# Kernel tuning notes

Measured on AMD Instinct MI355X. Metric: run time of the kernel, lower is better.

## Reference

```python
import jax, jax.numpy as jnp
import numpy as np

B, T, F = 4096, 256, 64
ANN_IN, OUT = 128, 32
U = [128, 128]


def setup_inputs() -> dict:
    key = jax.random.key(0)
    ks = jax.random.split(key, 8)
    s = 0.05  # weight scale for numerical sanity
    return {
        "inputs": jax.random.normal(ks[0], (B, T, F), jnp.float32),
        "W_in": jax.random.normal(ks[1], (F + OUT, ANN_IN), jnp.float32) * s,
        "b_in": jnp.zeros((ANN_IN,), jnp.float32),
        "k0": jax.random.normal(ks[2], (ANN_IN, 4 * U[0]), jnp.float32) * s,
        "rk0": jax.random.normal(ks[3], (U[0], 4 * U[0]), jnp.float32) * s,
        "bb0": jnp.zeros((4 * U[0],), jnp.float32),
        "k1": jax.random.normal(ks[4], (U[0], 4 * U[1]), jnp.float32) * s,
        "rk1": jax.random.normal(ks[5], (U[1], 4 * U[1]), jnp.float32) * s,
        "bb1": jnp.zeros((4 * U[1],), jnp.float32),
        "W_out": jax.random.normal(ks[6], (U[1], OUT), jnp.float32) * s,
        "b_out": jnp.zeros((OUT,), jnp.float32),
    }


def _lstm_cell(x, h, c, k, rk, b):
    # Keras LSTMCell: z = x@k + h@rk + b, split into i,f,g,o
    z = x @ k + h @ rk + b
    i, f, g, o = jnp.split(z, 4, axis=-1)
    c_new = jax.nn.sigmoid(f) * c + jax.nn.sigmoid(i) * jnp.tanh(g)
    h_new = jax.nn.sigmoid(o) * jnp.tanh(c_new)
    return h_new, c_new


def reference(inputs, W_in, b_in, k0, rk0, bb0, k1, rk1, bb1, W_out, b_out):
    b = inputs.shape[0]
    dt = inputs.dtype
    u0, u1 = rk0.shape[0], rk1.shape[0]
    out_units = W_out.shape[1]

    def step(carry, x_t):
        acc, h0, c0, h1, c1 = carry
        a = jnp.concatenate([x_t, acc], axis=-1) @ W_in + b_in  # ann_in Dense (linear)
        h0, c0 = _lstm_cell(a, h0, c0, k0, rk0, bb0)
        h1, c1 = _lstm_cell(h0, h1, c1, k1, rk1, bb1)
        res = h1 @ W_out + b_out  # ann_out Dense (linear)
        acc = acc + res  # explicit discrete integration
        return (acc, h0, c0, h1, c1), res

    init = (
        jnp.zeros((b, out_units), dt),
        jnp.zeros((b, u0), dt), jnp.zeros((b, u0), dt),
        jnp.zeros((b, u1), dt), jnp.zeros((b, u1), dt),
    )
    xs = jnp.swapaxes(inputs, 0, 1)  # [T, B, F]
    _, outs = jax.lax.scan(step, init, xs)
    return jnp.swapaxes(outs, 0, 1)  # [B, T, OUT] per-step residuals (cell outputs)
```

## Files before the change

kernel.cpp:

```cpp
#include <hip/hip_runtime.h>
#include <hip/hip_fp16.h>

typedef _Float16 half8  __attribute__((ext_vector_type(8)));
typedef _Float16 half2v __attribute__((ext_vector_type(2)));
typedef float    f32x4  __attribute__((ext_vector_type(4)));

#define MFMA16(af, bf, cf) __builtin_amdgcn_mfma_f32_16x16x32_f16((af), (bf), (cf), 0, 0, 0)

#define WS_WL1  0
#define WS_RK0  131072
#define WS_W0   (131072 + 65536)
#define WS_WOUT (WS_W0 + 49152)
#define WS_B0   (WS_WOUT + 4096)

#define PA0 104
#define PH  136
#define L_A0   0
#define L_H0   3328
#define L_H1   (L_H0 + 4352)
#define L_WOUT (L_H1 + 4352)
#define L_K1   (L_WOUT + 4096)
#define L_TOT  (L_K1 + 65536)

__device__ __forceinline__ float sigm(float x) {
    return __builtin_amdgcn_rcpf(1.0f + __builtin_amdgcn_exp2f(-1.442695041f * x));
}
__device__ __forceinline__ float tanh_(float x) {
    return 1.0f - 2.0f * __builtin_amdgcn_rcpf(__builtin_amdgcn_exp2f(2.885390082f * x) + 1.0f);
}
__device__ __forceinline__ void bar() {
    asm volatile("s_waitcnt lgkmcnt(0)" ::: "memory");
    __builtin_amdgcn_s_barrier();
    asm volatile("" ::: "memory");
}


__global__ void pack_layer_k(const float* __restrict__ kk, const float* __restrict__ rk,
                             _Float16* __restrict__ dst)
{
    int idx  = blockIdx.x * 256 + threadIdx.x;
    int j    = idx & 7;
    int lane = (idx >> 3) & 63;
    int fk   = idx >> 9;
    int kt   = fk & 7;
    int nt   = fk >> 3;
    int w = nt >> 3, ln = nt & 7, g = ln >> 1, hh = ln & 1;
    int col = g*128 + w*32 + hh*16 + (lane & 15);
    int row = kt*32 + (lane >> 4)*8 + j;
    float v = (row < 128) ? kk[row*512 + col] : rk[(row - 128)*512 + col];
    dst[idx] = (_Float16)v;
}

__global__ void pack_rk(const float* __restrict__ rk, _Float16* __restrict__ dst)
{
    int idx = blockIdx.x * 256 + threadIdx.x;
    int j = idx & 7, lane = (idx >> 3) & 63, fk = idx >> 9;
    int kt = fk & 3, nt = fk >> 2;
    int w = nt >> 3, ln = nt & 7, g = ln >> 1, hh = ln & 1;
    int col = g*128 + w*32 + hh*16 + (lane & 15);
    int row = kt*32 + (lane >> 4)*8 + j;
    dst[idx] = (_Float16)rk[row*512 + col];
}

__global__ void pack_w0(const float* __restrict__ W_in, const float* __restrict__ k0,
                        _Float16* __restrict__ dst)
{
    int idx = blockIdx.x * 256 + threadIdx.x;
    int j = idx & 7, lane = (idx >> 3) & 63, fk = idx >> 9;
    int kt = fk % 3, nt = fk / 3;
    int w = nt >> 3, ln = nt & 7, g = ln >> 1, hh = ln & 1;
    int col = g*128 + w*32 + hh*16 + (lane & 15);
    int row = kt*32 + (lane >> 4)*8 + j;
    float s = 0.f;
    #pragma unroll 4
    for (int k = 0; k < 128; ++k) s += W_in[row*128 + k] * k0[k*512 + col];
    dst[idx] = (_Float16)s;
}

__global__ void pack_b0(const float* __restrict__ b_in, const float* __restrict__ k0,
                        const float* __restrict__ bb0, float* __restrict__ b0p)
{
    int col = blockIdx.x * 256 + threadIdx.x;
    float s = bb0[col];
    #pragma unroll 4
    for (int k = 0; k < 128; ++k) s += b_in[k] * k0[k*512 + col];
    b0p[col] = s;
}

__global__ void pack_wout(const float* __restrict__ W_out, _Float16* __restrict__ dst)
{
    int idx = blockIdx.x * 256 + threadIdx.x;
    int j = idx & 7, lane = (idx >> 3) & 63, fk = idx >> 9;
    int kt = fk & 3, nt = fk >> 2;
    int col = nt*16 + (lane & 15);
    int row = kt*32 + (lane >> 4)*8 + j;
    dst[idx] = (_Float16)W_out[row*32 + col];
}

__global__ __launch_bounds__(512, 2)
void acclstm_main(const float* __restrict__ xin,
                  const _Float16* __restrict__ wl1p, const _Float16* __restrict__ rk0p,
                  const _Float16* __restrict__ w0p,  const _Float16* __restrict__ woutp,
                  const float* __restrict__ b0p, const float* __restrict__ bb1,
                  const float* __restrict__ bout, float* __restrict__ out)
{
    __shared__ __align__(16) _Float16 lds[L_TOT];
    const int tid  = threadIdx.x;
    const int W    = tid >> 6;
    const int lane = tid & 63;
    const int w4   = W & 3;
    const int hh   = W >> 2;
    const int l15  = lane & 15;
    const int lg   = lane >> 4;
    const int b0   = blockIdx.x << 4;
    const int colw = w4*32 + hh*16 + l15;

    for (int i = tid; i < 8192; i += 512) {
        int h = i << 3, nt = h >> 11, rem = h & 2047;
        *reinterpret_cast<uint4*>(&lds[L_K1 + h]) =
            *reinterpret_cast<const uint4*>(&wl1p[nt*4096 + rem]);
    }
    *reinterpret_cast<uint4*>(&lds[L_WOUT + (tid << 3)]) =
        *reinterpret_cast<const uint4*>(&woutp[tid << 3]);
    {
        uint4 z; z.x = z.y = z.z = z.w = 0u;
        for (int i = tid; i < 1504; i += 512)
            *reinterpret_cast<uint4*>(&lds[i << 3]) = z;
    }

    half8 w0r[4][3], rk0r[4][4], rk1r[4][4];
    #pragma unroll
    for (int g = 0; g < 4; ++g) {
        const int nt = w4*8 + g*2 + hh;
        #pragma unroll
        for (int kt = 0; kt < 3; ++kt)
            w0r[g][kt] = *reinterpret_cast<const half8*>(&w0p[(nt*3 + kt)*512 + lane*8]);
        #pragma unroll
        for (int kt = 0; kt < 4; ++kt)
            rk0r[g][kt] = *reinterpret_cast<const half8*>(&rk0p[(nt*4 + kt)*512 + lane*8]);
        #pragma unroll
        for (int kt = 0; kt < 4; ++kt)
            rk1r[g][kt] = *reinterpret_cast<const half8*>(&wl1p[(nt*8 + 4 + kt)*512 + lane*8]);
    }
    float b0v[4], b1v[4];
    #pragma unroll
    for (int g = 0; g < 4; ++g) {
        b0v[g] = b0p[g*128 + colw];
        b1v[g] = bb1[g*128 + colw];
    }
    const float boutv = (W < 2) ? bout[W*16 + l15] : 0.0f;

    f32x4 c0 = {0.f,0.f,0.f,0.f}, c1 = {0.f,0.f,0.f,0.f}, accv = {0.f,0.f,0.f,0.f};

    const int xrow = tid >> 5, xc2 = (tid & 31) << 1;
    __syncthreads();
    float2 xr = *reinterpret_cast<const float2*>(&xin[(size_t)(b0 + xrow)*16384 + xc2]);
    {
        half2v xh = { (_Float16)xr.x, (_Float16)xr.y };
        *reinterpret_cast<half2v*>(&lds[L_A0 + xrow*PA0 + xc2]) = xh;
    }
    xr = *reinterpret_cast<const float2*>(&xin[(size_t)(b0 + xrow)*16384 + 64 + xc2]);
    __syncthreads();

    auto step = [&](auto PARc, int t) {
        constexpr int PAR = decltype(PARc)::value;
        constexpr int A0r = L_A0 + PAR*1664,       A0w = L_A0 + (PAR^1)*1664;
        constexpr int H0r = L_H0 + PAR*2176,       H0w = L_H0 + (PAR^1)*2176;
        constexpr int H1r = L_H1 + PAR*2176,       H1w = L_H1 + (PAR^1)*2176;

        {
            f32x4 z0={0.f,0.f,0.f,0.f}, z1={0.f,0.f,0.f,0.f};
            f32x4 z2={0.f,0.f,0.f,0.f}, z3={0.f,0.f,0.f,0.f};
            #pragma unroll
            for (int kt = 0; kt < 3; ++kt) {
                half8 af = *reinterpret_cast<const half8*>(&lds[A0r + l15*PA0 + kt*32 + lg*8]);
                z0 = MFMA16(af, w0r[0][kt], z0);
                z1 = MFMA16(af, w0r[1][kt], z1);
                z2 = MFMA16(af, w0r[2][kt], z2);
                z3 = MFMA16(af, w0r[3][kt], z3);
            }
            #pragma unroll
            for (int kt = 0; kt < 4; ++kt) {
                half8 af = *reinterpret_cast<const half8*>(&lds[H0r + l15*PH + kt*32 + lg*8]);
                z0 = MFMA16(af, rk0r[0][kt], z0);
                z1 = MFMA16(af, rk0r[1][kt], z1);
                z2 = MFMA16(af, rk0r[2][kt], z2);
                z3 = MFMA16(af, rk0r[3][kt], z3);
            }
            #pragma unroll
            for (int r = 0; r < 4; ++r) {
                float iv = sigm (z0[r] + b0v[0]);
                float fv = sigm (z1[r] + b0v[1]);
                float gv = tanh_(z2[r] + b0v[2]);
                float ov = sigm (z3[r] + b0v[3]);
                float cn = fv * c0[r] + iv * gv;
                c0[r] = cn;
                lds[H0w + (lg*4 + r)*PH + colw] = (_Float16)(ov * tanh_(cn));
            }
        }
        bar();

        {
            f32x4 z0={0.f,0.f,0.f,0.f}, z1={0.f,0.f,0.f,0.f};
            f32x4 z2={0.f,0.f,0.f,0.f}, z3={0.f,0.f,0.f,0.f};
            #pragma unroll
            for (int kt = 0; kt < 4; ++kt) {
                half8 af = *reinterpret_cast<const half8*>(&lds[H0w + l15*PH + kt*32 + lg*8]);
                z0 = MFMA16(af, *reinterpret_cast<const half8*>(&lds[L_K1 + ((w4*8 + 0 + hh)*4 + kt)*512 + lane*8]), z0);
                z1 = MFMA16(af, *reinterpret_cast<const half8*>(&lds[L_K1 + ((w4*8 + 2 + hh)*4 + kt)*512 + lane*8]), z1);
                z2 = MFMA16(af, *reinterpret_cast<const half8*>(&lds[L_K1 + ((w4*8 + 4 + hh)*4 + kt)*512 + lane*8]), z2);
                z3 = MFMA16(af, *reinterpret_cast<const half8*>(&lds[L_K1 + ((w4*8 + 6 + hh)*4 + kt)*512 + lane*8]), z3);
            }
            #pragma unroll
            for (int kt = 0; kt < 4; ++kt) {
                half8 af = *reinterpret_cast<const half8*>(&lds[H1r + l15*PH + kt*32 + lg*8]);
                z0 = MFMA16(af, rk1r[0][kt], z0);
                z1 = MFMA16(af, rk1r[1][kt], z1);
                z2 = MFMA16(af, rk1r[2][kt], z2);
                z3 = MFMA16(af, rk1r[3][kt], z3);
            }
            #pragma unroll
            for (int r = 0; r < 4; ++r) {
                float iv = sigm (z0[r] + b1v[0]);
                float fv = sigm (z1[r] + b1v[1]);
                float gv = tanh_(z2[r] + b1v[2]);
                float ov = sigm (z3[r] + b1v[3]);
                float cn = fv * c1[r] + iv * gv;
                c1[r] = cn;
                lds[H1w + (lg*4 + r)*PH + colw] = (_Float16)(ov * tanh_(cn));
            }
        }
        bar();

        if (W < 2) {
            f32x4 rr = {0.f,0.f,0.f,0.f};
            #pragma unroll
            for (int kt = 0; kt < 4; ++kt) {
                half8 af = *reinterpret_cast<const half8*>(&lds[H1w + l15*PH + kt*32 + lg*8]);
                half8 wf = *reinterpret_cast<const half8*>(&lds[L_WOUT + (W*4 + kt)*512 + lane*8]);
                rr = MFMA16(af, wf, rr);
            }
            #pragma unroll
            for (int r = 0; r < 4; ++r) {
                float res = rr[r] + boutv;
                out[(size_t)(b0 + lg*4 + r)*8192 + t*32 + W*16 + l15] = res;
                accv[r] += res;
                lds[A0w + (lg*4 + r)*PA0 + 64 + W*16 + l15] = (_Float16)accv[r];
            }
        }
        {
            half2v xh = { (_Float16)xr.x, (_Float16)xr.y };
            *reinterpret_cast<half2v*>(&lds[A0w + xrow*PA0 + xc2]) = xh;
            int tn = t + 2; if (tn > 255) tn = 255;
            xr = *reinterpret_cast<const float2*>(&xin[(size_t)(b0 + xrow)*16384 + tn*64 + xc2]);
        }
        bar();
    };

    #pragma unroll 1
    for (int t = 0; t < 256; t += 2) {
        step(std::integral_constant<int,0>{}, t);
        step(std::integral_constant<int,1>{}, t + 1);
    }
}

extern "C" void kernel_launch(void* const* d_in, const int* in_sizes, int n_in,
                              void* d_out, int out_size, void* d_ws, size_t ws_size,
                              hipStream_t stream) {
    (void)in_sizes; (void)n_in; (void)out_size; (void)ws_size;
    const float* x     = (const float*)d_in[0];
    const float* W_in  = (const float*)d_in[1];
    const float* b_in  = (const float*)d_in[2];
    const float* k0    = (const float*)d_in[3];
    const float* rk0   = (const float*)d_in[4];
    const float* bb0   = (const float*)d_in[5];
    const float* k1    = (const float*)d_in[6];
    const float* rk1   = (const float*)d_in[7];
    const float* bb1   = (const float*)d_in[8];
    const float* W_out = (const float*)d_in[9];
    const float* b_out = (const float*)d_in[10];
    float* out = (float*)d_out;

    _Float16* ws    = (_Float16*)d_ws;
    _Float16* wl1p  = ws + WS_WL1;
    _Float16* rk0p  = ws + WS_RK0;
    _Float16* w0p   = ws + WS_W0;
    _Float16* woutp = ws + WS_WOUT;
    float*    b0p   = (float*)(ws + WS_B0);

    pack_layer_k<<<512, 256, 0, stream>>>(k1, rk1, wl1p);
    pack_rk     <<<256, 256, 0, stream>>>(rk0, rk0p);
    pack_w0     <<<192, 256, 0, stream>>>(W_in, k0, w0p);
    pack_b0     <<<2,   256, 0, stream>>>(b_in, k0, bb0, b0p);
    pack_wout   <<<16,  256, 0, stream>>>(W_out, woutp);
    acclstm_main<<<256, 512, 0, stream>>>(x, wl1p, rk0p, w0p, woutp,
                                          b0p, bb1, b_out, out);
}
```

Baseline: 780.5 us.

## Fold accumulator into layer-0 gate preactivation and merge output projection into layer 0 phase

```diff
diff --git a/kernel.cpp b/kernel.cpp
--- a/kernel.cpp
+++ b/kernel.cpp
@@ -7,20 +7,23 @@
 
 #define MFMA16(af, bf, cf) __builtin_amdgcn_mfma_f32_16x16x32_f16((af), (bf), (cf), 0, 0, 0)
 
-#define WS_WL1  0
-#define WS_RK0  131072
-#define WS_W0   (131072 + 65536)
-#define WS_WOUT (WS_W0 + 49152)
-#define WS_B0   (WS_WOUT + 4096)
-
-#define PA0 104
+#define WS_WL1   0
+#define WS_RK0   131072
+#define WS_W0    (131072 + 65536)
+#define WS_WOUTT (WS_W0 + 49152)
+#define WS_B0    (WS_WOUTT + 4096)
+#define WS_CB    (WS_B0 + 1024)
+
+#define PA0 72
 #define PH  136
-#define L_A0   0
-#define L_H0   3328
+#define PRES 40
+#define L_A0X  0
+#define L_H0   2304
 #define L_H1   (L_H0 + 4352)
-#define L_WOUT (L_H1 + 4352)
-#define L_K1   (L_WOUT + 4096)
-#define L_TOT  (L_K1 + 65536)
+#define L_RES  (L_H1 + 4352)
+#define L_WOUTT (L_RES + 5120)
+#define L_K1   (L_WOUTT + 4096)
+#define L_TOT  (L_K1 + 49152)
 
 __device__ __forceinline__ float sigm(float x) {
     return __builtin_amdgcn_rcpf(1.0f + __builtin_amdgcn_exp2f(-1.442695041f * x));
@@ -33,7 +36,6 @@
     __builtin_amdgcn_s_barrier();
     asm volatile("" ::: "memory");
 }
-
 
 __global__ void pack_layer_k(const float* __restrict__ kk, const float* __restrict__ rk,
                              _Float16* __restrict__ dst)
@@ -87,22 +89,37 @@
     b0p[col] = s;
 }
 
-__global__ void pack_wout(const float* __restrict__ W_out, _Float16* __restrict__ dst)
+__global__ void pack_woutT(const float* __restrict__ W_out, _Float16* __restrict__ dst)
 {
     int idx = blockIdx.x * 256 + threadIdx.x;
     int j = idx & 7, lane = (idx >> 3) & 63, fk = idx >> 9;
-    int kt = fk & 3, nt = fk >> 2;
-    int col = nt*16 + (lane & 15);
+    int kt = fk & 3, m = fk >> 2;
     int row = kt*32 + (lane >> 4)*8 + j;
+    int col = m*16 + (lane & 15);
     dst[idx] = (_Float16)W_out[row*32 + col];
+}
+
+__global__ void pack_cb(const float* __restrict__ W_in, const float* __restrict__ k0,
+                        const float* __restrict__ bout, float* __restrict__ cbp)
+{
+    int zc = blockIdx.x * 256 + threadIdx.x;
+    float s = 0.f;
+    for (int c = 0; c < 32; ++c) {
+        float wv = 0.f;
+        #pragma unroll 4
+        for (int k = 0; k < 128; ++k) wv += W_in[(64 + c)*128 + k] * k0[k*512 + zc];
+        s += bout[c] * wv;
+    }
+    cbp[zc] = s;
 }
 
 __global__ __launch_bounds__(512, 2)
 void acclstm_main(const float* __restrict__ xin,
                   const _Float16* __restrict__ wl1p, const _Float16* __restrict__ rk0p,
-                  const _Float16* __restrict__ w0p,  const _Float16* __restrict__ woutp,
-                  const float* __restrict__ b0p, const float* __restrict__ bb1,
-                  const float* __restrict__ bout, float* __restrict__ out)
+                  const _Float16* __restrict__ w0p,  const _Float16* __restrict__ woutTp,
+                  const float* __restrict__ b0p, const float* __restrict__ cbp,
+                  const float* __restrict__ bb1, const float* __restrict__ bout,
+                  float* __restrict__ out)
 {
     __shared__ __align__(16) _Float16 lds[L_TOT];
     const int tid  = threadIdx.x;
@@ -114,138 +131,136 @@
     const int lg   = lane >> 4;
     const int b0   = blockIdx.x << 4;
     const int colw = w4*32 + hh*16 + l15;
-
-    for (int i = tid; i < 8192; i += 512) {
-        int h = i << 3, nt = h >> 11, rem = h & 2047;
+    const int nt0 = w4*8 + 0 + hh, nt1 = w4*8 + 2 + hh, nt2 = w4*8 + 4 + hh, nt3 = w4*8 + 6 + hh;
+
+    for (int i = tid; i < 6144; i += 512) {
+        int h = i << 3, nt = h / 1536, rem = h % 1536;
         *reinterpret_cast<uint4*>(&lds[L_K1 + h]) =
             *reinterpret_cast<const uint4*>(&wl1p[nt*4096 + rem]);
     }
-    *reinterpret_cast<uint4*>(&lds[L_WOUT + (tid << 3)]) =
-        *reinterpret_cast<const uint4*>(&woutp[tid << 3]);
+    *reinterpret_cast<uint4*>(&lds[L_WOUTT + (tid << 3)]) =
+        *reinterpret_cast<const uint4*>(&woutTp[tid << 3]);
     {
         uint4 z; z.x = z.y = z.z = z.w = 0u;
-        for (int i = tid; i < 1504; i += 512)
-            *reinterpret_cast<uint4*>(&lds[i << 3]) = z;
-    }
-
-    half8 w0r[4][3], rk0r[4][4], rk1r[4][4];
+        if (tid < 272) {
+            *reinterpret_cast<uint4*>(&lds[L_H0 + (tid << 3)]) = z;
+            *reinterpret_cast<uint4*>(&lds[L_H1 + (tid << 3)]) = z;
+        }
+    }
+
+    half8 rk0r[4][4], rk1r[4][4], k1r[4], w0a[4];
+    {
+        const int nts[4] = {nt0, nt1, nt2, nt3};
+        #pragma unroll
+        for (int g = 0; g < 4; ++g) {
+            const int nt = nts[g];
+            #pragma unroll
+            for (int kt = 0; kt < 4; ++kt)
+                rk0r[g][kt] = *reinterpret_cast<const half8*>(&rk0p[(nt*4 + kt)*512 + lane*8]);
+            #pragma unroll
+            for (int kt = 0; kt < 4; ++kt)
+                rk1r[g][kt] = *reinterpret_cast<const half8*>(&wl1p[(nt*8 + 4 + kt)*512 + lane*8]);
+            k1r[g] = *reinterpret_cast<const half8*>(&wl1p[(nt*8 + 3)*512 + lane*8]);
+            w0a[g] = *reinterpret_cast<const half8*>(&w0p[(nt*3 + 2)*512 + lane*8]);
+        }
+    }
+    float b1v[4], cbv[4];
+    f32x4 za[4];
     #pragma unroll
     for (int g = 0; g < 4; ++g) {
-        const int nt = w4*8 + g*2 + hh;
-        #pragma unroll
-        for (int kt = 0; kt < 3; ++kt)
-            w0r[g][kt] = *reinterpret_cast<const half8*>(&w0p[(nt*3 + kt)*512 + lane*8]);
-        #pragma unroll
-        for (int kt = 0; kt < 4; ++kt)
-            rk0r[g][kt] = *reinterpret_cast<const half8*>(&rk0p[(nt*4 + kt)*512 + lane*8]);
-        #pragma unroll
-        for (int kt = 0; kt < 4; ++kt)
-            rk1r[g][kt] = *reinterpret_cast<const half8*>(&wl1p[(nt*8 + 4 + kt)*512 + lane*8]);
-    }
-    float b0v[4], b1v[4];
+        b1v[g] = bb1[g*128 + colw];
+        cbv[g] = cbp[g*128 + colw];
+        float z0i = b0p[g*128 + colw] - cbv[g];
+        za[g] = (f32x4){z0i, z0i, z0i, z0i};
+    }
+    float boutv4[4];
     #pragma unroll
-    for (int g = 0; g < 4; ++g) {
-        b0v[g] = b0p[g*128 + colw];
-        b1v[g] = bb1[g*128 + colw];
-    }
-    const float boutv = (W < 2) ? bout[W*16 + l15] : 0.0f;
-
-    f32x4 c0 = {0.f,0.f,0.f,0.f}, c1 = {0.f,0.f,0.f,0.f}, accv = {0.f,0.f,0.f,0.f};
+    for (int r = 0; r < 4; ++r)
+        boutv4[r] = bout[(W < 2 ? W : 0)*16 + lg*4 + r];
+
+    f32x4 c0 = {0.f,0.f,0.f,0.f}, c1 = {0.f,0.f,0.f,0.f};
 
     const int xrow = tid >> 5, xc2 = (tid & 31) << 1;
+    const int resw = L_RES + W*640 + l15*PRES;
+
     __syncthreads();
     float2 xr = *reinterpret_cast<const float2*>(&xin[(size_t)(b0 + xrow)*16384 + xc2]);
     {
         half2v xh = { (_Float16)xr.x, (_Float16)xr.y };
-        *reinterpret_cast<half2v*>(&lds[L_A0 + xrow*PA0 + xc2]) = xh;
+        *reinterpret_cast<half2v*>(&lds[L_A0X + xrow*PA0 + xc2]) = xh;
     }
     xr = *reinterpret_cast<const float2*>(&xin[(size_t)(b0 + xrow)*16384 + 64 + xc2]);
     __syncthreads();
 
     auto step = [&](auto PARc, int t) {
         constexpr int PAR = decltype(PARc)::value;
-        constexpr int A0r = L_A0 + PAR*1664,       A0w = L_A0 + (PAR^1)*1664;
-        constexpr int H0r = L_H0 + PAR*2176,       H0w = L_H0 + (PAR^1)*2176;
-        constexpr int H1r = L_H1 + PAR*2176,       H1w = L_H1 + (PAR^1)*2176;
+        constexpr int A0r = L_A0X + PAR*1152, A0w = L_A0X + (PAR^1)*1152;
+        constexpr int H0r = L_H0 + PAR*2176,  H0w = L_H0 + (PAR^1)*2176;
+        constexpr int H1r = L_H1 + PAR*2176,  H1w = L_H1 + (PAR^1)*2176;
 
         {
-            f32x4 z0={0.f,0.f,0.f,0.f}, z1={0.f,0.f,0.f,0.f};
-            f32x4 z2={0.f,0.f,0.f,0.f}, z3={0.f,0.f,0.f,0.f};
-            #pragma unroll
-            for (int kt = 0; kt < 3; ++kt) {
-                half8 af = *reinterpret_cast<const half8*>(&lds[A0r + l15*PA0 + kt*32 + lg*8]);
-                z0 = MFMA16(af, w0r[0][kt], z0);
-                z1 = MFMA16(af, w0r[1][kt], z1);
-                z2 = MFMA16(af, w0r[2][kt], z2);
-                z3 = MFMA16(af, w0r[3][kt], z3);
-            }
+            f32x4 rr0 = {0.f,0.f,0.f,0.f}, rr1 = {0.f,0.f,0.f,0.f};
             #pragma unroll
             for (int kt = 0; kt < 4; ++kt) {
-                half8 af = *reinterpret_cast<const half8*>(&lds[H0r + l15*PH + kt*32 + lg*8]);
-                z0 = MFMA16(af, rk0r[0][kt], z0);
-                z1 = MFMA16(af, rk0r[1][kt], z1);
-                z2 = MFMA16(af, rk0r[2][kt], z2);
-                z3 = MFMA16(af, rk0r[3][kt], z3);
+                half8 hf  = *reinterpret_cast<const half8*>(&lds[H1r + l15*PH + kt*32 + lg*8]);
+                half8 wt0 = *reinterpret_cast<const half8*>(&lds[L_WOUTT + (0*4 + kt)*512 + lane*8]);
+                half8 wt1 = *reinterpret_cast<const half8*>(&lds[L_WOUTT + (1*4 + kt)*512 + lane*8]);
+                rr0 = MFMA16(wt0, hf, rr0);
+                rr1 = MFMA16(wt1, hf, rr1);
             }
             #pragma unroll
             for (int r = 0; r < 4; ++r) {
-                float iv = sigm (z0[r] + b0v[0]);
-                float fv = sigm (z1[r] + b0v[1]);
-                float gv = tanh_(z2[r] + b0v[2]);
-                float ov = sigm (z3[r] + b0v[3]);
+                lds[resw + lg*4 + r]      = (_Float16)rr0[r];
+                lds[resw + 16 + lg*4 + r] = (_Float16)rr1[r];
+            }
+            asm volatile("s_waitcnt lgkmcnt(0)" ::: "memory");
+            half8 resA = *reinterpret_cast<const half8*>(&lds[resw + lg*8]);
+            #pragma unroll
+            for (int g = 0; g < 4; ++g) {
+                za[g] = MFMA16(resA, w0a[g], za[g]);
+                #pragma unroll
+                for (int r = 0; r < 4; ++r) za[g][r] += cbv[g];
+            }
+            if (t && W < 2) {
+                const f32x4& rrs = (W == 0) ? rr0 : rr1;
+                #pragma unroll
+                for (int r = 0; r < 4; ++r)
+                    out[(size_t)(b0 + l15)*8192 + (t-1)*32 + W*16 + lg*4 + r] = rrs[r] + boutv4[r];
+            }
+        }
+
+        {
+            half8 ax0 = *reinterpret_cast<const half8*>(&lds[A0r + l15*PA0 +  0 + lg*8]);
+            half8 ax1 = *reinterpret_cast<const half8*>(&lds[A0r + l15*PA0 + 32 + lg*8]);
+            half8 wx00 = *reinterpret_cast<const half8*>(&w0p[(nt0*3 + 0)*512 + lane*8]);
+            half8 wx01 = *reinterpret_cast<const half8*>(&w0p[(nt0*3 + 1)*512 + lane*8]);
+            half8 wx10 = *reinterpret_cast<const half8*>(&w0p[(nt1*3 + 0)*512 + lane*8]);
+            half8 wx11 = *reinterpret_cast<const half8*>(&w0p[(nt1*3 + 1)*512 + lane*8]);
+            half8 wx20 = *reinterpret_cast<const half8*>(&w0p[(nt2*3 + 0)*512 + lane*8]);
+            half8 wx21 = *reinterpret_cast<const half8*>(&w0p[(nt2*3 + 1)*512 + lane*8]);
+            half8 wx30 = *reinterpret_cast<const half8*>(&w0p[(nt3*3 + 0)*512 + lane*8]);
+            half8 wx31 = *reinterpret_cast<const half8*>(&w0p[(nt3*3 + 1)*512 + lane*8]);
+            f32x4 z0 = MFMA16(ax0, wx00, za[0]); z0 = MFMA16(ax1, wx01, z0);
+            f32x4 z1 = MFMA16(ax0, wx10, za[1]); z1 = MFMA16(ax1, wx11, z1);
+            f32x4 z2 = MFMA16(ax0, wx20, za[2]); z2 = MFMA16(ax1, wx21, z2);
+            f32x4 z3 = MFMA16(ax0, wx30, za[3]); z3 = MFMA16(ax1, wx31, z3);
+            #pragma unroll
+            for (int kt = 0; kt < 4; ++kt) {
+                half8 hf = *reinterpret_cast<const half8*>(&lds[H0r + l15*PH + kt*32 + lg*8]);
+                z0 = MFMA16(hf, rk0r[0][kt], z0);
+                z1 = MFMA16(hf, rk0r[1][kt], z1);
+                z2 = MFMA16(hf, rk0r[2][kt], z2);
+                z3 = MFMA16(hf, rk0r[3][kt], z3);
+            }
+            #pragma unroll
+            for (int r = 0; r < 4; ++r) {
+                float iv = sigm (z0[r]);
+                float fv = sigm (z1[r]);
+                float gv = tanh_(z2[r]);
+                float ov = sigm (z3[r]);
                 float cn = fv * c0[r] + iv * gv;
                 c0[r] = cn;
                 lds[H0w + (lg*4 + r)*PH + colw] = (_Float16)(ov * tanh_(cn));
-            }
-        }
-        bar();
-
-        {
-            f32x4 z0={0.f,0.f,0.f,0.f}, z1={0.f,0.f,0.f,0.f};
-            f32x4 z2={0.f,0.f,0.f,0.f}, z3={0.f,0.f,0.f,0.f};
-            #pragma unroll
-            for (int kt = 0; kt < 4; ++kt) {
-                half8 af = *reinterpret_cast<const half8*>(&lds[H0w + l15*PH + kt*32 + lg*8]);
-                z0 = MFMA16(af, *reinterpret_cast<const half8*>(&lds[L_K1 + ((w4*8 + 0 + hh)*4 + kt)*512 + lane*8]), z0);
-                z1 = MFMA16(af, *reinterpret_cast<const half8*>(&lds[L_K1 + ((w4*8 + 2 + hh)*4 + kt)*512 + lane*8]), z1);
-                z2 = MFMA16(af, *reinterpret_cast<const half8*>(&lds[L_K1 + ((w4*8 + 4 + hh)*4 + kt)*512 + lane*8]), z2);
-                z3 = MFMA16(af, *reinterpret_cast<const half8*>(&lds[L_K1 + ((w4*8 + 6 + hh)*4 + kt)*512 + lane*8]), z3);
-            }
-            #pragma unroll
-            for (int kt = 0; kt < 4; ++kt) {
-                half8 af = *reinterpret_cast<const half8*>(&lds[H1r + l15*PH + kt*32 + lg*8]);
-                z0 = MFMA16(af, rk1r[0][kt], z0);
-                z1 = MFMA16(af, rk1r[1][kt], z1);
-                z2 = MFMA16(af, rk1r[2][kt], z2);
-                z3 = MFMA16(af, rk1r[3][kt], z3);
-            }
-            #pragma unroll
-            for (int r = 0; r < 4; ++r) {
-                float iv = sigm (z0[r] + b1v[0]);
-                float fv = sigm (z1[r] + b1v[1]);
-                float gv = tanh_(z2[r] + b1v[2]);
-                float ov = sigm (z3[r] + b1v[3]);
-                float cn = fv * c1[r] + iv * gv;
-                c1[r] = cn;
-                lds[H1w + (lg*4 + r)*PH + colw] = (_Float16)(ov * tanh_(cn));
-            }
-        }
-        bar();
-
-        if (W < 2) {
-            f32x4 rr = {0.f,0.f,0.f,0.f};
-            #pragma unroll
-            for (int kt = 0; kt < 4; ++kt) {
-                half8 af = *reinterpret_cast<const half8*>(&lds[H1w + l15*PH + kt*32 + lg*8]);
-                half8 wf = *reinterpret_cast<const half8*>(&lds[L_WOUT + (W*4 + kt)*512 + lane*8]);
-                rr = MFMA16(af, wf, rr);
-            }
-            #pragma unroll
-            for (int r = 0; r < 4; ++r) {
-                float res = rr[r] + boutv;
-                out[(size_t)(b0 + lg*4 + r)*8192 + t*32 + W*16 + l15] = res;
-                accv[r] += res;
-                lds[A0w + (lg*4 + r)*PA0 + 64 + W*16 + l15] = (_Float16)accv[r];
             }
         }
         {
@@ -255,12 +270,71 @@
             xr = *reinterpret_cast<const float2*>(&xin[(size_t)(b0 + xrow)*16384 + tn*64 + xc2]);
         }
         bar();
+
+        {
+            f32x4 z0 = {b1v[0],b1v[0],b1v[0],b1v[0]};
+            f32x4 z1 = {b1v[1],b1v[1],b1v[1],b1v[1]};
+            f32x4 z2 = {b1v[2],b1v[2],b1v[2],b1v[2]};
+            f32x4 z3 = {b1v[3],b1v[3],b1v[3],b1v[3]};
+            #pragma unroll
+            for (int kt = 0; kt < 3; ++kt) {
+                half8 hf = *reinterpret_cast<const half8*>(&lds[H0w + l15*PH + kt*32 + lg*8]);
+                z0 = MFMA16(hf, *reinterpret_cast<const half8*>(&lds[L_K1 + (nt0*3 + kt)*512 + lane*8]), z0);
+                z1 = MFMA16(hf, *reinterpret_cast<const half8*>(&lds[L_K1 + (nt1*3 + kt)*512 + lane*8]), z1);
+                z2 = MFMA16(hf, *reinterpret_cast<const half8*>(&lds[L_K1 + (nt2*3 + kt)*512 + lane*8]), z2);
+                z3 = MFMA16(hf, *reinterpret_cast<const half8*>(&lds[L_K1 + (nt3*3 + kt)*512 + lane*8]), z3);
+            }
+            {
+                half8 hf = *reinterpret_cast<const half8*>(&lds[H0w + l15*PH + 3*32 + lg*8]);
+                z0 = MFMA16(hf, k1r[0], z0);
+                z1 = MFMA16(hf, k1r[1], z1);
+                z2 = MFMA16(hf, k1r[2], z2);
+                z3 = MFMA16(hf, k1r[3], z3);
+            }
+            #pragma unroll
+            for (int kt = 0; kt < 4; ++kt) {
+                half8 hf = *reinterpret_cast<const half8*>(&lds[H1r + l15*PH + kt*32 + lg*8]);
+                z0 = MFMA16(hf, rk1r[0][kt], z0);
+                z1 = MFMA16(hf, rk1r[1][kt], z1);
+                z2 = MFMA16(hf, rk1r[2][kt], z2);
+                z3 = MFMA16(hf, rk1r[3][kt], z3);
+            }
+            #pragma unroll
+            for (int r = 0; r < 4; ++r) {
+                float iv = sigm (z0[r]);
+                float fv = sigm (z1[r]);
+                float gv = tanh_(z2[r]);
+                float ov = sigm (z3[r]);
+                float cn = fv * c1[r] + iv * gv;
+                c1[r] = cn;
+                lds[H1w + (lg*4 + r)*PH + colw] = (_Float16)(ov * tanh_(cn));
+            }
+        }
+        bar();
     };
 
     #pragma unroll 1
     for (int t = 0; t < 256; t += 2) {
         step(std::integral_constant<int,0>{}, t);
         step(std::integral_constant<int,1>{}, t + 1);
+    }
+
+    {
+        f32x4 rr0 = {0.f,0.f,0.f,0.f}, rr1 = {0.f,0.f,0.f,0.f};
+        #pragma unroll
+        for (int kt = 0; kt < 4; ++kt) {
+            half8 hf  = *reinterpret_cast<const half8*>(&lds[L_H1 + l15*PH + kt*32 + lg*8]);
+            half8 wt0 = *reinterpret_cast<const half8*>(&lds[L_WOUTT + (0*4 + kt)*512 + lane*8]);
+            half8 wt1 = *reinterpret_cast<const half8*>(&lds[L_WOUTT + (1*4 + kt)*512 + lane*8]);
+            rr0 = MFMA16(wt0, hf, rr0);
+            rr1 = MFMA16(wt1, hf, rr1);
+        }
+        if (W < 2) {
+            const f32x4& rrs = (W == 0) ? rr0 : rr1;
+            #pragma unroll
+            for (int r = 0; r < 4; ++r)
+                out[(size_t)(b0 + l15)*8192 + 255*32 + W*16 + lg*4 + r] = rrs[r] + boutv4[r];
+        }
     }
 }
 
@@ -281,18 +355,20 @@
     const float* b_out = (const float*)d_in[10];
     float* out = (float*)d_out;
 
-    _Float16* ws    = (_Float16*)d_ws;
-    _Float16* wl1p  = ws + WS_WL1;
-    _Float16* rk0p  = ws + WS_RK0;
-    _Float16* w0p   = ws + WS_W0;
-    _Float16* woutp = ws + WS_WOUT;
-    float*    b0p   = (float*)(ws + WS_B0);
+    _Float16* ws     = (_Float16*)d_ws;
+    _Float16* wl1p   = ws + WS_WL1;
+    _Float16* rk0p   = ws + WS_RK0;
+    _Float16* w0p    = ws + WS_W0;
+    _Float16* woutTp = ws + WS_WOUTT;
+    float*    b0p    = (float*)(ws + WS_B0);
+    float*    cbp    = (float*)(ws + WS_CB);
 
     pack_layer_k<<<512, 256, 0, stream>>>(k1, rk1, wl1p);
     pack_rk     <<<256, 256, 0, stream>>>(rk0, rk0p);
     pack_w0     <<<192, 256, 0, stream>>>(W_in, k0, w0p);
     pack_b0     <<<2,   256, 0, stream>>>(b_in, k0, bb0, b0p);
-    pack_wout   <<<16,  256, 0, stream>>>(W_out, woutp);
-    acclstm_main<<<256, 512, 0, stream>>>(x, wl1p, rk0p, w0p, woutp,
-                                          b0p, bb1, b_out, out);
-}
+    pack_woutT  <<<16,  256, 0, stream>>>(W_out, woutTp);
+    pack_cb     <<<2,   256, 0, stream>>>(W_in, k0, b_out, cbp);
+    acclstm_main<<<256, 512, 0, stream>>>(x, wl1p, rk0p, w0p, woutTp,
+                                          b0p, cbp, bb1, b_out, out);
+}
```

New measurement: 1.575 ms. 2.02x slower.

## Load inputs directly into MFMA fragments and shrink LDS staging to acc

Applied to the files above, without the earlier changes.

```diff
diff --git a/kernel.cpp b/kernel.cpp
--- a/kernel.cpp
+++ b/kernel.cpp
@@ -2,7 +2,6 @@
 #include <hip/hip_fp16.h>
 
 typedef _Float16 half8  __attribute__((ext_vector_type(8)));
-typedef _Float16 half2v __attribute__((ext_vector_type(2)));
 typedef float    f32x4  __attribute__((ext_vector_type(4)));
 
 #define MFMA16(af, bf, cf) __builtin_amdgcn_mfma_f32_16x16x32_f16((af), (bf), (cf), 0, 0, 0)
@@ -13,10 +12,10 @@
 #define WS_WOUT (WS_W0 + 49152)
 #define WS_B0   (WS_WOUT + 4096)
 
-#define PA0 104
-#define PH  136
-#define L_A0   0
-#define L_H0   3328
+#define PACC 40
+#define PH   136
+#define L_ACC  0
+#define L_H0   1280
 #define L_H1   (L_H0 + 4352)
 #define L_WOUT (L_H1 + 4352)
 #define L_K1   (L_WOUT + 4096)
@@ -33,7 +32,6 @@
     __builtin_amdgcn_s_barrier();
     asm volatile("" ::: "memory");
 }
-
 
 __global__ void pack_layer_k(const float* __restrict__ kk, const float* __restrict__ rk,
                              _Float16* __restrict__ dst)
@@ -124,17 +122,21 @@
         *reinterpret_cast<const uint4*>(&woutp[tid << 3]);
     {
         uint4 z; z.x = z.y = z.z = z.w = 0u;
-        for (int i = tid; i < 1504; i += 512)
-            *reinterpret_cast<uint4*>(&lds[i << 3]) = z;
-    }
-
-    half8 w0r[4][3], rk0r[4][4], rk1r[4][4];
+        if (tid < 272) {
+            *reinterpret_cast<uint4*>(&lds[L_H0 + (tid << 3)]) = z;
+            *reinterpret_cast<uint4*>(&lds[L_H1 + (tid << 3)]) = z;
+        }
+        if (tid < 160)
+            *reinterpret_cast<uint4*>(&lds[L_ACC + (tid << 3)]) = z;
+    }
+
+    half8 w0r[4][2], w0a[4], rk0r[4][4], rk1r[4][4];
     #pragma unroll
     for (int g = 0; g < 4; ++g) {
         const int nt = w4*8 + g*2 + hh;
-        #pragma unroll
-        for (int kt = 0; kt < 3; ++kt)
-            w0r[g][kt] = *reinterpret_cast<const half8*>(&w0p[(nt*3 + kt)*512 + lane*8]);
+        w0r[g][0] = *reinterpret_cast<const half8*>(&w0p[(nt*3 + 0)*512 + lane*8]);
+        w0r[g][1] = *reinterpret_cast<const half8*>(&w0p[(nt*3 + 1)*512 + lane*8]);
+        w0a[g]    = *reinterpret_cast<const half8*>(&w0p[(nt*3 + 2)*512 + lane*8]);
         #pragma unroll
         for (int kt = 0; kt < 4; ++kt)
             rk0r[g][kt] = *reinterpret_cast<const half8*>(&rk0p[(nt*4 + kt)*512 + lane*8]);
@@ -152,47 +154,51 @@
 
     f32x4 c0 = {0.f,0.f,0.f,0.f}, c1 = {0.f,0.f,0.f,0.f}, accv = {0.f,0.f,0.f,0.f};
 
-    const int xrow = tid >> 5, xc2 = (tid & 31) << 1;
-    __syncthreads();
-    float2 xr = *reinterpret_cast<const float2*>(&xin[(size_t)(b0 + xrow)*16384 + xc2]);
-    {
-        half2v xh = { (_Float16)xr.x, (_Float16)xr.y };
-        *reinterpret_cast<half2v*>(&lds[L_A0 + xrow*PA0 + xc2]) = xh;
-    }
-    xr = *reinterpret_cast<const float2*>(&xin[(size_t)(b0 + xrow)*16384 + 64 + xc2]);
+    const float* xrow = xin + (size_t)(b0 + l15)*16384 + lg*8;
+    float4 xq0, xq1, xq2, xq3;
+    xq0 = *reinterpret_cast<const float4*>(xrow + 0);
+    xq1 = *reinterpret_cast<const float4*>(xrow + 4);
+    xq2 = *reinterpret_cast<const float4*>(xrow + 32);
+    xq3 = *reinterpret_cast<const float4*>(xrow + 36);
+
     __syncthreads();
 
     auto step = [&](auto PARc, int t) {
         constexpr int PAR = decltype(PARc)::value;
-        constexpr int A0r = L_A0 + PAR*1664,       A0w = L_A0 + (PAR^1)*1664;
-        constexpr int H0r = L_H0 + PAR*2176,       H0w = L_H0 + (PAR^1)*2176;
-        constexpr int H1r = L_H1 + PAR*2176,       H1w = L_H1 + (PAR^1)*2176;
+        constexpr int ACCr = L_ACC + PAR*640, ACCw = L_ACC + (PAR^1)*640;
+        constexpr int H0r = L_H0 + PAR*2176,  H0w = L_H0 + (PAR^1)*2176;
+        constexpr int H1r = L_H1 + PAR*2176,  H1w = L_H1 + (PAR^1)*2176;
 
         {
-            f32x4 z0={0.f,0.f,0.f,0.f}, z1={0.f,0.f,0.f,0.f};
-            f32x4 z2={0.f,0.f,0.f,0.f}, z3={0.f,0.f,0.f,0.f};
-            #pragma unroll
-            for (int kt = 0; kt < 3; ++kt) {
-                half8 af = *reinterpret_cast<const half8*>(&lds[A0r + l15*PA0 + kt*32 + lg*8]);
-                z0 = MFMA16(af, w0r[0][kt], z0);
-                z1 = MFMA16(af, w0r[1][kt], z1);
-                z2 = MFMA16(af, w0r[2][kt], z2);
-                z3 = MFMA16(af, w0r[3][kt], z3);
-            }
+            half8 aac = *reinterpret_cast<const half8*>(&lds[ACCr + l15*PACC + lg*8]);
+            f32x4 z0 = {b0v[0],b0v[0],b0v[0],b0v[0]};
+            f32x4 z1 = {b0v[1],b0v[1],b0v[1],b0v[1]};
+            f32x4 z2 = {b0v[2],b0v[2],b0v[2],b0v[2]};
+            f32x4 z3 = {b0v[3],b0v[3],b0v[3],b0v[3]};
             #pragma unroll
             for (int kt = 0; kt < 4; ++kt) {
-                half8 af = *reinterpret_cast<const half8*>(&lds[H0r + l15*PH + kt*32 + lg*8]);
-                z0 = MFMA16(af, rk0r[0][kt], z0);
-                z1 = MFMA16(af, rk0r[1][kt], z1);
-                z2 = MFMA16(af, rk0r[2][kt], z2);
-                z3 = MFMA16(af, rk0r[3][kt], z3);
-            }
+                half8 hf = *reinterpret_cast<const half8*>(&lds[H0r + l15*PH + kt*32 + lg*8]);
+                z0 = MFMA16(hf, rk0r[0][kt], z0);
+                z1 = MFMA16(hf, rk0r[1][kt], z1);
+                z2 = MFMA16(hf, rk0r[2][kt], z2);
+                z3 = MFMA16(hf, rk0r[3][kt], z3);
+            }
+            half8 ax0 = { (_Float16)xq0.x, (_Float16)xq0.y, (_Float16)xq0.z, (_Float16)xq0.w,
+                          (_Float16)xq1.x, (_Float16)xq1.y, (_Float16)xq1.z, (_Float16)xq1.w };
+            half8 ax1 = { (_Float16)xq2.x, (_Float16)xq2.y, (_Float16)xq2.z, (_Float16)xq2.w,
+                          (_Float16)xq3.x, (_Float16)xq3.y, (_Float16)xq3.z, (_Float16)xq3.w };
+            z0 = MFMA16(ax0, w0r[0][0], z0); z1 = MFMA16(ax0, w0r[1][0], z1);
+            z2 = MFMA16(ax0, w0r[2][0], z2); z3 = MFMA16(ax0, w0r[3][0], z3);
+            z0 = MFMA16(ax1, w0r[0][1], z0); z1 = MFMA16(ax1, w0r[1][1], z1);
+            z2 = MFMA16(ax1, w0r[2][1], z2); z3 = MFMA16(ax1, w0r[3][1], z3);
+            z0 = MFMA16(aac, w0a[0], z0);    z1 = MFMA16(aac, w0a[1], z1);
+            z2 = MFMA16(aac, w0a[2], z2);    z3 = MFMA16(aac, w0a[3], z3);
             #pragma unroll
             for (int r = 0; r < 4; ++r) {
-                float iv = sigm (z0[r] + b0v[0]);
-                float fv = sigm (z1[r] + b0v[1]);
-                float gv = tanh_(z2[r] + b0v[2]);
-                float ov = sigm (z3[r] + b0v[3]);
+                float iv = sigm (z0[r]);
+                float fv = sigm (z1[r]);
+                float gv = tanh_(z2[r]);
+                float ov = sigm (z3[r]);
                 float cn = fv * c0[r] + iv * gv;
                 c0[r] = cn;
                 lds[H0w + (lg*4 + r)*PH + colw] = (_Float16)(ov * tanh_(cn));
@@ -201,30 +207,32 @@
         bar();
 
         {
-            f32x4 z0={0.f,0.f,0.f,0.f}, z1={0.f,0.f,0.f,0.f};
-            f32x4 z2={0.f,0.f,0.f,0.f}, z3={0.f,0.f,0.f,0.f};
+            f32x4 z0 = {b1v[0],b1v[0],b1v[0],b1v[0]};
+            f32x4 z1 = {b1v[1],b1v[1],b1v[1],b1v[1]};
+            f32x4 z2 = {b1v[2],b1v[2],b1v[2],b1v[2]};
+            f32x4 z3 = {b1v[3],b1v[3],b1v[3],b1v[3]};
             #pragma unroll
             for (int kt = 0; kt < 4; ++kt) {
-                half8 af = *reinterpret_cast<const half8*>(&lds[H0w + l15*PH + kt*32 + lg*8]);
-                z0 = MFMA16(af, *reinterpret_cast<const half8*>(&lds[L_K1 + ((w4*8 + 0 + hh)*4 + kt)*512 + lane*8]), z0);
-                z1 = MFMA16(af, *reinterpret_cast<const half8*>(&lds[L_K1 + ((w4*8 + 2 + hh)*4 + kt)*512 + lane*8]), z1);
-                z2 = MFMA16(af, *reinterpret_cast<const half8*>(&lds[L_K1 + ((w4*8 + 4 + hh)*4 + kt)*512 + lane*8]), z2);
-                z3 = MFMA16(af, *reinterpret_cast<const half8*>(&lds[L_K1 + ((w4*8 + 6 + hh)*4 + kt)*512 + lane*8]), z3);
+                half8 hf = *reinterpret_cast<const half8*>(&lds[H0w + l15*PH + kt*32 + lg*8]);
+                z0 = MFMA16(hf, *reinterpret_cast<const half8*>(&lds[L_K1 + ((w4*8 + 0 + hh)*4 + kt)*512 + lane*8]), z0);
+                z1 = MFMA16(hf, *reinterpret_cast<const half8*>(&lds[L_K1 + ((w4*8 + 2 + hh)*4 + kt)*512 + lane*8]), z1);
+                z2 = MFMA16(hf, *reinterpret_cast<const half8*>(&lds[L_K1 + ((w4*8 + 4 + hh)*4 + kt)*512 + lane*8]), z2);
+                z3 = MFMA16(hf, *reinterpret_cast<const half8*>(&lds[L_K1 + ((w4*8 + 6 + hh)*4 + kt)*512 + lane*8]), z3);
             }
             #pragma unroll
             for (int kt = 0; kt < 4; ++kt) {
-                half8 af = *reinterpret_cast<const half8*>(&lds[H1r + l15*PH + kt*32 + lg*8]);
-                z0 = MFMA16(af, rk1r[0][kt], z0);
-                z1 = MFMA16(af, rk1r[1][kt], z1);
-                z2 = MFMA16(af, rk1r[2][kt], z2);
-                z3 = MFMA16(af, rk1r[3][kt], z3);
+                half8 hf = *reinterpret_cast<const half8*>(&lds[H1r + l15*PH + kt*32 + lg*8]);
+                z0 = MFMA16(hf, rk1r[0][kt], z0);
+                z1 = MFMA16(hf, rk1r[1][kt], z1);
+                z2 = MFMA16(hf, rk1r[2][kt], z2);
+                z3 = MFMA16(hf, rk1r[3][kt], z3);
             }
             #pragma unroll
             for (int r = 0; r < 4; ++r) {
-                float iv = sigm (z0[r] + b1v[0]);
-                float fv = sigm (z1[r] + b1v[1]);
-                float gv = tanh_(z2[r] + b1v[2]);
-                float ov = sigm (z3[r] + b1v[3]);
+                float iv = sigm (z0[r]);
+                float fv = sigm (z1[r]);
+                float gv = tanh_(z2[r]);
+                float ov = sigm (z3[r]);
                 float cn = fv * c1[r] + iv * gv;
                 c1[r] = cn;
                 lds[H1w + (lg*4 + r)*PH + colw] = (_Float16)(ov * tanh_(cn));
@@ -232,8 +240,16 @@
         }
         bar();
 
+        {
+            const int tn = (t < 255) ? (t + 1) : t;
+            const float* xb = xrow + tn*64;
+            xq0 = *reinterpret_cast<const float4*>(xb + 0);
+            xq1 = *reinterpret_cast<const float4*>(xb + 4);
+            xq2 = *reinterpret_cast<const float4*>(xb + 32);
+            xq3 = *reinterpret_cast<const float4*>(xb + 36);
+        }
         if (W < 2) {
-            f32x4 rr = {0.f,0.f,0.f,0.f};
+            f32x4 rr = {boutv,boutv,boutv,boutv};
             #pragma unroll
             for (int kt = 0; kt < 4; ++kt) {
                 half8 af = *reinterpret_cast<const half8*>(&lds[H1w + l15*PH + kt*32 + lg*8]);
@@ -242,17 +258,11 @@
             }
             #pragma unroll
             for (int r = 0; r < 4; ++r) {
-                float res = rr[r] + boutv;
+                float res = rr[r];
                 out[(size_t)(b0 + lg*4 + r)*8192 + t*32 + W*16 + l15] = res;
                 accv[r] += res;
-                lds[A0w + (lg*4 + r)*PA0 + 64 + W*16 + l15] = (_Float16)accv[r];
-            }
-        }
-        {
-            half2v xh = { (_Float16)xr.x, (_Float16)xr.y };
-            *reinterpret_cast<half2v*>(&lds[A0w + xrow*PA0 + xc2]) = xh;
-            int tn = t + 2; if (tn > 255) tn = 255;
-            xr = *reinterpret_cast<const float2*>(&xin[(size_t)(b0 + xrow)*16384 + tn*64 + xc2]);
+                lds[ACCw + (lg*4 + r)*PACC + W*16 + l15] = (_Float16)accv[r];
+            }
         }
         bar();
     };
```

After: 1.248 ms. +59.9%, slower.
